# Kernel tuning notes

Measured on AMD Instinct MI355X. Metric: run time of the kernel, lower is better.

The kernel has to match this reference:

```python
import jax, jax.numpy as jnp
import numpy as np

B, S, D, A = 8, 4096, 128, 128


def _pos_encoding(seq_len, dim):
    # sin/cos positional encoding, same construction as the torch buffer
    pos = np.arange(seq_len, dtype=np.float32)[:, None]
    div = np.exp(np.arange(0, dim, 2, dtype=np.float32) * (-np.log(10000.0) / dim))
    pe = np.zeros((seq_len, dim), dtype=np.float32)
    pe[:, 0::2] = np.sin(pos * div)
    pe[:, 1::2] = np.cos(pos * div)
    return jnp.asarray(pe)


def setup_inputs() -> dict:
    key = jax.random.key(0)
    ks = jax.random.split(key, 7)
    sc = 1.0 / np.sqrt(D)
    return {
        "x": jax.random.normal(ks[0], (B, S, D), dtype=jnp.float32),
        "Wq": jax.random.normal(ks[1], (D, A), dtype=jnp.float32) * sc,
        "bq": jnp.zeros((A,), dtype=jnp.float32),
        "Wk": jax.random.normal(ks[2], (D, A), dtype=jnp.float32) * sc,
        "bk": jnp.zeros((A,), dtype=jnp.float32),
        "Wv": jax.random.normal(ks[3], (D, A), dtype=jnp.float32) * sc,
        "bv": jnp.zeros((A,), dtype=jnp.float32),
    }


def reference(x, Wq, bq, Wk, bk, Wv, bv):
    b, s, d = x.shape
    pe = _pos_encoding(s, d)  # [S, D]
    xp = x + pe[None]  # broadcast add of positional encoding
    q = xp @ Wq + bq  # [B, S, A]
    k = xp @ Wk + bk
    v = xp @ Wv + bv
    scale = 1.0 / jnp.sqrt(jnp.asarray(Wq.shape[1], dtype=jnp.float32))
    scores = jnp.einsum("bsa,bta->bst", q, k) * scale  # [B, S, S]
    weights = jax.nn.softmax(scores, axis=-1)
    out = jnp.einsum("bst,bta->bsa", weights, v)  # [B, S, A]
    return out
```

## Files before the change

### kernel.cpp

```cpp
#include <hip/hip_runtime.h>

#define BB 8
#define SS 4096
#define DD 128

typedef __attribute__((ext_vector_type(8))) short v8s;
typedef __attribute__((ext_vector_type(4))) float v4f;
typedef __attribute__((ext_vector_type(16))) float v16f;

__device__ __forceinline__ unsigned short f2bf(float f) {
    unsigned int u = __float_as_uint(f);
    u += 0x7fffu + ((u >> 16) & 1u);
    return (unsigned short)(u >> 16);
}
__device__ __forceinline__ unsigned int pk_bf16(float a, float b) {
    unsigned int ua = __float_as_uint(a) + 0x8000u;
    unsigned int ub = __float_as_uint(b) + 0x8000u;
    return __builtin_amdgcn_perm(ub, ua, 0x07060302u);
}

#if !defined(__HIP_DEVICE_COMPILE__)
#define MFMA16(a, b, c) (c)
#define MFMA32(a, b, c) (c)
#define GLDS16(g, l)
#define WAITVM(n)
#define WAITLGKM()
#define BAR()
#else
#define MFMA16(a, b, c) __builtin_amdgcn_mfma_f32_16x16x32_bf16((a), (b), (c), 0, 0, 0)
#define MFMA32(a, b, c) __builtin_amdgcn_mfma_f32_32x32x16_bf16((a), (b), (c), 0, 0, 0)
#define GLDS16(g, l)                                                         \
    __builtin_amdgcn_global_load_lds(                                        \
        (const __attribute__((address_space(1))) unsigned int*)(g),          \
        (__attribute__((address_space(3))) unsigned int*)(l), 16, 0, 0)
#define WAITVM(n) asm volatile("s_waitcnt vmcnt(" #n ")" ::: "memory")
#define WAITLGKM() asm volatile("s_waitcnt lgkmcnt(0)" ::: "memory")
#define BAR()                                                                \
    do {                                                                     \
        asm volatile("" ::: "memory");                                       \
        __builtin_amdgcn_s_barrier();                                        \
        __builtin_amdgcn_sched_barrier(0);                                   \
        asm volatile("" ::: "memory");                                       \
    } while (0)
#endif

#if !defined(__HIP_DEVICE_COMPILE__)
#define EXP2F(x) exp2f(x)
#elif __has_builtin(__builtin_amdgcn_exp2f)
#define EXP2F(x) __builtin_amdgcn_exp2f(x)
#else
#define EXP2F(x) exp2f(x)
#endif

#define QSCALE 0.12751743f

__global__ __launch_bounds__(256) void prep_kernel(
    const float* __restrict__ Wq, const float* __restrict__ Wk,
    const float* __restrict__ Wv, unsigned short* __restrict__ Wt)
{
    int id = blockIdx.x * 256 + threadIdx.x;
    int w = id >> 14;
    int n = (id >> 7) & 127;
    int k = id & 127;
    const float* W = (w == 0) ? Wq : (w == 1) ? Wk : Wv;
    Wt[id] = f2bf(W[k * 128 + n]);
}

__global__ __launch_bounds__(256, 3) void proj_kernel(
    const float* __restrict__ x, const unsigned short* __restrict__ Wt,
    const float* __restrict__ bq, const float* __restrict__ bk,
    const float* __restrict__ bv,
    unsigned short* __restrict__ qo, unsigned short* __restrict__ ko,
    unsigned short* __restrict__ vo)
{
    __shared__ __attribute__((aligned(16))) unsigned short w_lds[128 * 136];
    __shared__ __attribute__((aligned(16))) unsigned short o_lds[9216];

    const int tid = threadIdx.x;
    const int wave = tid >> 6;
    const int lane = tid & 63;
    const int quad = lane >> 4;
    const int l15 = lane & 15;
    const int bid = blockIdx.x;
    const int mat = bid % 3;
    const int rbase = (bid / 3) * 64;

    const unsigned short* Wp = Wt + (mat << 14);
#pragma unroll
    for (int it = 0; it < 8; ++it) {
        int id = it * 256 + tid;
        int n = id >> 4, c8 = id & 15;
        *(v8s*)(w_lds + n * 136 + c8 * 8) = *(const v8s*)(Wp + n * 128 + c8 * 8);
    }

    const int flatrow = rbase + wave * 16 + l15;
    const int srow = flatrow & 4095;
    v8s af[4];
#pragma unroll
    for (int kc = 0; kc < 4; ++kc) {
        const int kbase = kc * 32 + quad * 8;
        const v4f* xp = (const v4f*)(x + (size_t)flatrow * DD + kbase);
        v4f x0 = xp[0], x1 = xp[1];
        float p[8];
#pragma unroll
        for (int j = 0; j < 8; j += 2) {
            float freq = __expf((float)(kbase + j) * -0.07195578415606394f);
            float arg = (float)srow * freq;
            p[j] = __sinf(arg);
            p[j + 1] = __cosf(arg);
        }
        v8s a;
#pragma unroll
        for (int j = 0; j < 4; ++j) a[j] = (short)f2bf(x0[j] + p[j]);
#pragma unroll
        for (int j = 0; j < 4; ++j) a[4 + j] = (short)f2bf(x1[j] + p[4 + j]);
        af[kc] = a;
    }

    const float* bias = (mat == 0) ? bq : (mat == 1) ? bk : bv;
    const int quadp = ((quad & 1) << 1) | (quad >> 1);
    __syncthreads();

#pragma unroll
    for (int nb = 0; nb < 8; ++nb) {
        const int col = nb * 16 + l15;
        v4f acc = {0.f, 0.f, 0.f, 0.f};
#pragma unroll
        for (int kc = 0; kc < 4; ++kc) {
            v8s bf = *(const v8s*)(w_lds + col * 136 + kc * 32 + quad * 8);
            acc = MFMA16(af[kc], bf, acc);
        }
        float bval = bias[col];
#pragma unroll
        for (int reg = 0; reg < 4; ++reg) {
            float val = acc[reg] + bval;
            if (mat == 0) {
                int lr = wave * 16 + quad * 4 + reg;
                o_lds[lr * 136 + col] = f2bf(val * QSCALE);
            } else if (mat == 1) {
                int lr = wave * 16 + quad * 4 + reg;
                o_lds[lr * 136 + col] = f2bf(val);
            } else {
                int plr = wave * 16 + quadp * 4 + reg;
                o_lds[col * 72 + plr] = f2bf(val);
            }
        }
    }
    __syncthreads();

    if (mat <= 1) {
        unsigned short* outp = (mat == 0) ? qo : ko;
#pragma unroll
        for (int it = 0; it < 4; ++it) {
            int id = it * 256 + tid;
            int r = id >> 4, c8 = id & 15;
            *(v8s*)(outp + (size_t)(rbase + r) * DD + c8 * 8) =
                *(const v8s*)(o_lds + r * 136 + c8 * 8);
        }
    } else {
        const int b0 = rbase >> 12, s0 = rbase & 4095;
#pragma unroll
        for (int it = 0; it < 4; ++it) {
            int id = it * 256 + tid;
            int a = id >> 3, c = id & 7;
            *(v8s*)(vo + ((size_t)(b0 * 128 + a)) * SS + s0 + c * 8) =
                *(const v8s*)(o_lds + a * 72 + c * 8);
        }
    }
}

#define HKEYS 2048
#define NT 32
__global__ __launch_bounds__(512, 2) void flash_kernel(
    const unsigned short* __restrict__ qp,
    const unsigned short* __restrict__ kp,
    const unsigned short* __restrict__ vp,
    float* __restrict__ outp)
{
    __shared__ __attribute__((aligned(16))) unsigned short k_lds[2][2][8192];
    __shared__ __attribute__((aligned(16))) unsigned short v_lds[2][2][8192];
    __shared__ float xl[8][32];

    const int tid = threadIdx.x;
    const int wave = tid >> 6;
    const int lane = tid & 63;
    const int hi = lane >> 5;
    const int l31 = lane & 31;
    const int half = wave >> 2;
    const int qs = wave & 3;
    const int wv = wave & 3;
    const int bid = blockIdx.x;
    const int b = bid & 7;
    const int qt = bid >> 3;
    const int qbase = qt * 128;

    const size_t qrow = (size_t)(b * SS + qbase + qs * 32 + l31) * DD;
    v8s qf[8];
#pragma unroll
    for (int kc = 0; kc < 8; ++kc)
        qf[kc] = *(const v8s*)(qp + qrow + kc * 16 + hi * 8);

    v16f o[4];
#pragma unroll
    for (int fg = 0; fg < 4; ++fg)
#pragma unroll
        for (int r = 0; r < 16; ++r) o[fg][r] = 0.f;
    float lp = 0.f;

    const int kro = half * 32768 + l31 * 256 + ((hi ^ (l31 & 15)) << 4);
    const int vro = half * 32768 + l31 * 128 + (((l31 & 7) ^ hi) << 4);

    const int krow = wv * 4 + (lane >> 4);
    const unsigned short* ksrc =
        kp + ((size_t)(b * SS + half * HKEYS) + krow) * DD +
        (((lane & 15) ^ krow) << 3);
    const int vrow = lane >> 3;
    const unsigned short* vsrc =
        vp + (size_t)b * DD * SS + (size_t)(wv * 8 + vrow) * SS + half * HKEYS +
        (((lane & 7) ^ vrow) << 3);
    unsigned short* kd0 = &k_lds[half][0][wv * 512];
    unsigned short* vd0 = &v_lds[half][0][wv * 512];

    auto stage = [&](int p, int t) {
        unsigned short* kd = kd0 + p * 8192;
        unsigned short* vd = vd0 + p * 8192;
        const unsigned short* ks = ksrc + (size_t)t * 64 * DD;
        const unsigned short* vs = vsrc + t * 64;
#pragma unroll
        for (int it = 0; it < 4; ++it)
            GLDS16(ks + (size_t)it * 16 * DD, kd + it * 2048);
#pragma unroll
        for (int it = 0; it < 4; ++it)
            GLDS16(vs + (size_t)it * 32 * SS, vd + it * 2048);
    };

    auto compute = [&](int p, int sub) {
        const int ka = kro + p * 16384 + sub * 8192;
        v16f s;
#pragma unroll
        for (int r = 0; r < 16; ++r) s[r] = 0.f;
#pragma unroll
        for (int kc = 0; kc < 8; ++kc) {
            v8s af = *(const v8s*)((const char*)k_lds + (ka ^ (kc << 5)));
            s = MFMA32(af, qf[kc], s);
        }
        float e[16];
#pragma unroll
        for (int r = 0; r < 16; ++r) e[r] = EXP2F(s[r]);
        lp += (((e[0] + e[1]) + (e[2] + e[3])) + ((e[4] + e[5]) + (e[6] + e[7]))) +
              (((e[8] + e[9]) + (e[10] + e[11])) + ((e[12] + e[13]) + (e[14] + e[15])));
        union { v8s v[2]; unsigned int u[8]; } P;
#pragma unroll
        for (int g = 0; g < 2; ++g)
#pragma unroll
            for (int m = 0; m < 4; ++m)
                P.u[g * 4 + m] = pk_bf16(e[2 * m + 8 * g], e[2 * m + 8 * g + 1]);
        const int vb2 = (vro + p * 16384) ^ (sub << 6);
#pragma unroll
        for (int g = 0; g < 2; ++g) {
            const int vg = vb2 ^ (g << 5);
#pragma unroll
            for (int fg = 0; fg < 4; ++fg) {
                v8s bf = *(const v8s*)((const char*)v_lds + (vg + fg * 4096));
                o[fg] = MFMA32(P.v[g], bf, o[fg]);
            }
        }
    };

    stage(0, 0);
#pragma unroll 1
    for (int t = 0; t < NT; t += 2) {
        stage(1, t + 1);
        WAITVM(8);
        BAR();
        compute(0, 0);
        compute(0, 1);
        WAITLGKM();
        BAR();
        if (t + 2 < NT) {
            stage(0, t + 2);
            WAITVM(8);
        } else {
            WAITVM(0);
        }
        BAR();
        compute(1, 0);
        compute(1, 1);
        WAITLGKM();
        BAR();
    }

    lp += __shfl_xor(lp, 32);
    if (hi == 0) xl[wave][l31] = lp;

    float* kf = (float*)&k_lds[0][0][0];

    auto putO = [&](float* base) {
#pragma unroll
        for (int fg = 0; fg < 4; ++fg) {
            v4f* bp = (v4f*)(base + fg * 1024 + lane * 16);
#pragma unroll
            for (int c = 0; c < 4; ++c) {
                v4f tv = {o[fg][c * 4 + 0], o[fg][c * 4 + 1],
                          o[fg][c * 4 + 2], o[fg][c * 4 + 3]};
                bp[c ^ (lane & 3)] = tv;
            }
        }
    };
    auto addO = [&](const float* base) {
#pragma unroll
        for (int fg = 0; fg < 4; ++fg) {
            const v4f* bp = (const v4f*)(base + fg * 1024 + lane * 16);
#pragma unroll
            for (int c = 0; c < 4; ++c) {
                v4f tv = bp[c ^ (lane & 3)];
#pragma unroll
                for (int j = 0; j < 4; ++j) o[fg][c * 4 + j] += tv[j];
            }
        }
    };

    if (half == 1) putO(kf + qs * 4096);
    __syncthreads();
    if (half == 0) {
        addO(kf + qs * 4096);
        float ir[16];
#pragma unroll
        for (int r = 0; r < 16; ++r) {
            int qr = (r & 3) + 8 * (r >> 2) + 4 * hi;
            ir[r] = 1.0f / (xl[qs][qr] + xl[4 + qs][qr]);
        }
#pragma unroll
        for (int fg = 0; fg < 4; ++fg)
#pragma unroll
            for (int r = 0; r < 16; ++r) {
                int qr = (r & 3) + 8 * (r >> 2) + 4 * hi;
                outp[(size_t)(b * SS + qbase + qs * 32 + qr) * DD +
                     fg * 32 + l31] = o[fg][r] * ir[r];
            }
    }
}

extern "C" void kernel_launch(void* const* d_in, const int* in_sizes, int n_in,
                              void* d_out, int out_size, void* d_ws, size_t ws_size,
                              hipStream_t stream)
{
    const float* x  = (const float*)d_in[0];
    const float* Wq = (const float*)d_in[1];
    const float* bq = (const float*)d_in[2];
    const float* Wk = (const float*)d_in[3];
    const float* bk = (const float*)d_in[4];
    const float* Wv = (const float*)d_in[5];
    const float* bv = (const float*)d_in[6];
    float* out = (float*)d_out;

    unsigned short* Wt = (unsigned short*)d_ws;
    unsigned short* q  = Wt + 49152;
    unsigned short* k  = q + (size_t)BB * SS * DD;
    unsigned short* vT = k + (size_t)BB * SS * DD;

    hipLaunchKernelGGL(prep_kernel, dim3(192), dim3(256), 0, stream,
                       Wq, Wk, Wv, Wt);
    hipLaunchKernelGGL(proj_kernel, dim3(BB * SS / 64 * 3), dim3(256), 0, stream,
                       x, Wt, bq, bk, bv, q, k, vT);
    hipLaunchKernelGGL(flash_kernel, dim3(BB * SS / 128), dim3(512), 0, stream,
                       q, k, vT, out);
}
```

Measured before the change: 167.8 us.

## Fuse weight prep, QKV projection and flash attention into one kernel with grid barrier

Merges the three kernels into a single persistent launch. Each block projects its own 128 rows of Q, K and V, reading fp32 weights directly and transposing them into LDS. Q stays in swizzled LDS and is never written to global memory. K and V go to the workspace, and a software grid-wide atomic barrier makes them visible before attention starts. This removes launch gaps and the Q round-trip, but every block now repeats the weight conversion, and the barrier depends on all 256 blocks being co-resident.

```diff
diff --git a/kernel.cpp b/kernel.cpp
--- a/kernel.cpp
+++ b/kernel.cpp
@@ -54,151 +54,154 @@
 
 #define QSCALE 0.12751743f
 
-__global__ __launch_bounds__(256) void prep_kernel(
-    const float* __restrict__ Wq, const float* __restrict__ Wk,
-    const float* __restrict__ Wv, unsigned short* __restrict__ Wt)
-{
-    int id = blockIdx.x * 256 + threadIdx.x;
-    int w = id >> 14;
-    int n = (id >> 7) & 127;
-    int k = id & 127;
-    const float* W = (w == 0) ? Wq : (w == 1) ? Wk : Wv;
-    Wt[id] = f2bf(W[k * 128 + n]);
-}
-
-__global__ __launch_bounds__(256, 3) void proj_kernel(
-    const float* __restrict__ x, const unsigned short* __restrict__ Wt,
-    const float* __restrict__ bq, const float* __restrict__ bk,
-    const float* __restrict__ bv,
-    unsigned short* __restrict__ qo, unsigned short* __restrict__ ko,
-    unsigned short* __restrict__ vo)
-{
-    __shared__ __attribute__((aligned(16))) unsigned short w_lds[128 * 136];
-    __shared__ __attribute__((aligned(16))) unsigned short o_lds[9216];
-
-    const int tid = threadIdx.x;
-    const int wave = tid >> 6;
-    const int lane = tid & 63;
-    const int quad = lane >> 4;
-    const int l15 = lane & 15;
-    const int bid = blockIdx.x;
-    const int mat = bid % 3;
-    const int rbase = (bid / 3) * 64;
-
-    const unsigned short* Wp = Wt + (mat << 14);
-#pragma unroll
-    for (int it = 0; it < 8; ++it) {
-        int id = it * 256 + tid;
-        int n = id >> 4, c8 = id & 15;
-        *(v8s*)(w_lds + n * 136 + c8 * 8) = *(const v8s*)(Wp + n * 128 + c8 * 8);
-    }
-
-    const int flatrow = rbase + wave * 16 + l15;
-    const int srow = flatrow & 4095;
-    v8s af[4];
-#pragma unroll
-    for (int kc = 0; kc < 4; ++kc) {
-        const int kbase = kc * 32 + quad * 8;
-        const v4f* xp = (const v4f*)(x + (size_t)flatrow * DD + kbase);
-        v4f x0 = xp[0], x1 = xp[1];
-        float p[8];
-#pragma unroll
-        for (int j = 0; j < 8; j += 2) {
-            float freq = __expf((float)(kbase + j) * -0.07195578415606394f);
-            float arg = (float)srow * freq;
-            p[j] = __sinf(arg);
-            p[j + 1] = __cosf(arg);
-        }
-        v8s a;
-#pragma unroll
-        for (int j = 0; j < 4; ++j) a[j] = (short)f2bf(x0[j] + p[j]);
-#pragma unroll
-        for (int j = 0; j < 4; ++j) a[4 + j] = (short)f2bf(x1[j] + p[4 + j]);
-        af[kc] = a;
-    }
-
-    const float* bias = (mat == 0) ? bq : (mat == 1) ? bk : bv;
-    const int quadp = ((quad & 1) << 1) | (quad >> 1);
-    __syncthreads();
-
-#pragma unroll
-    for (int nb = 0; nb < 8; ++nb) {
-        const int col = nb * 16 + l15;
-        v4f acc = {0.f, 0.f, 0.f, 0.f};
-#pragma unroll
-        for (int kc = 0; kc < 4; ++kc) {
-            v8s bf = *(const v8s*)(w_lds + col * 136 + kc * 32 + quad * 8);
-            acc = MFMA16(af[kc], bf, acc);
-        }
-        float bval = bias[col];
-#pragma unroll
-        for (int reg = 0; reg < 4; ++reg) {
-            float val = acc[reg] + bval;
-            if (mat == 0) {
-                int lr = wave * 16 + quad * 4 + reg;
-                o_lds[lr * 136 + col] = f2bf(val * QSCALE);
-            } else if (mat == 1) {
-                int lr = wave * 16 + quad * 4 + reg;
-                o_lds[lr * 136 + col] = f2bf(val);
-            } else {
-                int plr = wave * 16 + quadp * 4 + reg;
-                o_lds[col * 72 + plr] = f2bf(val);
-            }
-        }
-    }
-    __syncthreads();
-
-    if (mat <= 1) {
-        unsigned short* outp = (mat == 0) ? qo : ko;
-#pragma unroll
-        for (int it = 0; it < 4; ++it) {
-            int id = it * 256 + tid;
-            int r = id >> 4, c8 = id & 15;
-            *(v8s*)(outp + (size_t)(rbase + r) * DD + c8 * 8) =
-                *(const v8s*)(o_lds + r * 136 + c8 * 8);
-        }
-    } else {
-        const int b0 = rbase >> 12, s0 = rbase & 4095;
-#pragma unroll
-        for (int it = 0; it < 4; ++it) {
-            int id = it * 256 + tid;
-            int a = id >> 3, c = id & 7;
-            *(v8s*)(vo + ((size_t)(b0 * 128 + a)) * SS + s0 + c * 8) =
-                *(const v8s*)(o_lds + a * 72 + c * 8);
-        }
-    }
-}
-
 #define HKEYS 2048
 #define NT 32
-__global__ __launch_bounds__(512, 2) void flash_kernel(
-    const unsigned short* __restrict__ qp,
-    const unsigned short* __restrict__ kp,
-    const unsigned short* __restrict__ vp,
-    float* __restrict__ outp)
+__global__ __launch_bounds__(512, 2) void fused_kernel(
+    const float* __restrict__ x,
+    const float* __restrict__ Wq, const float* __restrict__ bq,
+    const float* __restrict__ Wk, const float* __restrict__ bk,
+    const float* __restrict__ Wv, const float* __restrict__ bv,
+    unsigned short* __restrict__ ko, unsigned short* __restrict__ vo,
+    float* __restrict__ outp, unsigned int* bar)
 {
     __shared__ __attribute__((aligned(16))) unsigned short k_lds[2][2][8192];
     __shared__ __attribute__((aligned(16))) unsigned short v_lds[2][2][8192];
-    __shared__ float xl[8][32];
+    __shared__ __attribute__((aligned(16))) unsigned short q_lds[16384];
 
     const int tid = threadIdx.x;
     const int wave = tid >> 6;
     const int lane = tid & 63;
     const int hi = lane >> 5;
     const int l31 = lane & 31;
-    const int half = wave >> 2;
-    const int qs = wave & 3;
-    const int wv = wave & 3;
     const int bid = blockIdx.x;
     const int b = bid & 7;
     const int qt = bid >> 3;
     const int qbase = qt * 128;
 
-    const size_t qrow = (size_t)(b * SS + qbase + qs * 32 + l31) * DD;
+    {
+        const int quad = lane >> 4;
+        const int l15 = lane & 15;
+        const int xrow = qbase + wave * 16 + l15;
+
+        v8s af[4];
+#pragma unroll
+        for (int kc = 0; kc < 4; ++kc) {
+            const int kbase = kc * 32 + quad * 8;
+            const v4f* xp = (const v4f*)(x + (size_t)(b * SS + xrow) * DD + kbase);
+            v4f x0 = xp[0], x1 = xp[1];
+            float p[8];
+#pragma unroll
+            for (int j = 0; j < 8; j += 2) {
+                float freq = __expf((float)(kbase + j) * -0.07195578415606394f);
+                float arg = (float)xrow * freq;
+                p[j] = __sinf(arg);
+                p[j + 1] = __cosf(arg);
+            }
+            v8s a;
+#pragma unroll
+            for (int j = 0; j < 4; ++j) a[j] = (short)f2bf(x0[j] + p[j]);
+#pragma unroll
+            for (int j = 0; j < 4; ++j) a[4 + j] = (short)f2bf(x1[j] + p[4 + j]);
+            af[kc] = a;
+        }
+
+        unsigned short* w_lds = &k_lds[0][0][0];
+        unsigned short* o_lds = &v_lds[0][0][0];
+        const int quadp = ((quad & 1) << 1) | (quad >> 1);
+
+#pragma unroll 1
+        for (int m = 0; m < 3; ++m) {
+            const float* W = (m == 0) ? Wq : (m == 1) ? Wk : Wv;
+            const float* bias = (m == 0) ? bq : (m == 1) ? bk : bv;
+            __syncthreads();
+#pragma unroll
+            for (int j = 0; j < 32; ++j) {
+                int id = j * 512 + tid;
+                int n = id >> 7, k2 = id & 127;
+                w_lds[n * 136 + k2] = f2bf(W[k2 * 128 + n]);
+            }
+            __syncthreads();
+
+#pragma unroll
+            for (int nb = 0; nb < 8; ++nb) {
+                const int col = nb * 16 + l15;
+                v4f acc = {0.f, 0.f, 0.f, 0.f};
+#pragma unroll
+                for (int kc = 0; kc < 4; ++kc) {
+                    v8s bf = *(const v8s*)(w_lds + col * 136 + kc * 32 + quad * 8);
+                    acc = MFMA16(af[kc], bf, acc);
+                }
+                float bval = bias[col];
+#pragma unroll
+                for (int reg = 0; reg < 4; ++reg) {
+                    float val = acc[reg] + bval;
+                    if (m == 0) {
+                        int row = wave * 16 + quad * 4 + reg;
+                        int boff = row * 256 + ((col * 2) ^ ((row & 7) << 4));
+                        *(unsigned short*)((char*)q_lds + boff) =
+                            f2bf(val * QSCALE);
+                    } else if (m == 1) {
+                        int lr = wave * 16 + quad * 4 + reg;
+                        o_lds[lr * 136 + col] = f2bf(val);
+                    } else {
+                        int plr = wave * 16 + quadp * 4 + reg;
+                        o_lds[col * 136 + plr] = f2bf(val);
+                    }
+                }
+            }
+            if (m == 1) {
+                __syncthreads();
+#pragma unroll
+                for (int it = 0; it < 4; ++it) {
+                    int id = it * 512 + tid;
+                    int r = id >> 4, c8 = id & 15;
+                    *(v8s*)(ko + (size_t)(b * SS + qbase + r) * DD + c8 * 8) =
+                        *(const v8s*)(o_lds + r * 136 + c8 * 8);
+                }
+            } else if (m == 2) {
+                __syncthreads();
+#pragma unroll
+                for (int it = 0; it < 4; ++it) {
+                    int id = it * 512 + tid;
+                    int a = id >> 4, c = id & 15;
+                    *(v8s*)(vo + (size_t)(b * DD + a) * SS + qbase + c * 8) =
+                        *(const v8s*)(o_lds + a * 136 + c * 8);
+                }
+            }
+        }
+    }
+
+    WAITVM(0);
+    __syncthreads();
+    if (tid == 0) {
+        __threadfence();
+        unsigned int gen = __hip_atomic_load(&bar[1], __ATOMIC_RELAXED,
+                                             __HIP_MEMORY_SCOPE_AGENT);
+        unsigned int old = __hip_atomic_fetch_add(&bar[0], 1u, __ATOMIC_ACQ_REL,
+                                                  __HIP_MEMORY_SCOPE_AGENT);
+        if (old == 255u) {
+            __hip_atomic_store(&bar[0], 0u, __ATOMIC_RELAXED,
+                               __HIP_MEMORY_SCOPE_AGENT);
+            __hip_atomic_fetch_add(&bar[1], 1u, __ATOMIC_ACQ_REL,
+                                   __HIP_MEMORY_SCOPE_AGENT);
+        } else {
+            while (__hip_atomic_load(&bar[1], __ATOMIC_ACQUIRE,
+                                     __HIP_MEMORY_SCOPE_AGENT) == gen) {}
+        }
+        __threadfence();
+    }
+    __syncthreads();
+
+    const int half = wave >> 2;
+    const int qs = wave & 3;
+    const int wv = wave & 3;
+
+    const int qrow2 = qs * 32 + l31;
+    const char* qlp = (const char*)q_lds + qrow2 * 256;
     v8s qf[8];
 #pragma unroll
     for (int kc = 0; kc < 8; ++kc)
-        qf[kc] = *(const v8s*)(qp + qrow + kc * 16 + hi * 8);
+        qf[kc] = *(const v8s*)(qlp + (((2 * kc + hi) ^ (qrow2 & 7)) << 4));
 
     v16f o[4];
 #pragma unroll
@@ -212,11 +215,11 @@
 
     const int krow = wv * 4 + (lane >> 4);
     const unsigned short* ksrc =
-        kp + ((size_t)(b * SS + half * HKEYS) + krow) * DD +
+        ko + ((size_t)(b * SS + half * HKEYS) + krow) * DD +
         (((lane & 15) ^ krow) << 3);
     const int vrow = lane >> 3;
     const unsigned short* vsrc =
-        vp + (size_t)b * DD * SS + (size_t)(wv * 8 + vrow) * SS + half * HKEYS +
+        vo + (size_t)b * DD * SS + (size_t)(wv * 8 + vrow) * SS + half * HKEYS +
         (((lane & 7) ^ vrow) << 3);
     unsigned short* kd0 = &k_lds[half][0][wv * 512];
     unsigned short* vd0 = &v_lds[half][0][wv * 512];
@@ -291,7 +294,8 @@
     }
 
     lp += __shfl_xor(lp, 32);
-    if (hi == 0) xl[wave][l31] = lp;
+    float* xl = (float*)q_lds;
+    if (hi == 0) xl[wave * 32 + l31] = lp;
 
     float* kf = (float*)&k_lds[0][0][0];
 
@@ -328,7 +332,7 @@
 #pragma unroll
         for (int r = 0; r < 16; ++r) {
             int qr = (r & 3) + 8 * (r >> 2) + 4 * hi;
-            ir[r] = 1.0f / (xl[qs][qr] + xl[4 + qs][qr]);
+            ir[r] = 1.0f / (xl[qs * 32 + qr] + xl[(4 + qs) * 32 + qr]);
         }
 #pragma unroll
         for (int fg = 0; fg < 4; ++fg)
@@ -354,15 +358,11 @@
     const float* bv = (const float*)d_in[6];
     float* out = (float*)d_out;
 
-    unsigned short* Wt = (unsigned short*)d_ws;
-    unsigned short* q  = Wt + 49152;
-    unsigned short* k  = q + (size_t)BB * SS * DD;
-    unsigned short* vT = k + (size_t)BB * SS * DD;
-
-    hipLaunchKernelGGL(prep_kernel, dim3(192), dim3(256), 0, stream,
-                       Wq, Wk, Wv, Wt);
-    hipLaunchKernelGGL(proj_kernel, dim3(BB * SS / 64 * 3), dim3(256), 0, stream,
-                       x, Wt, bq, bk, bv, q, k, vT);
-    hipLaunchKernelGGL(flash_kernel, dim3(BB * SS / 128), dim3(512), 0, stream,
-                       q, k, vT, out);
+    unsigned short* ko = (unsigned short*)d_ws;
+    unsigned short* vo = ko + (size_t)BB * SS * DD;
+    unsigned int* bar = (unsigned int*)(vo + (size_t)BB * SS * DD);
+
+    hipMemsetAsync(bar, 0, 8, stream);
+    hipLaunchKernelGGL(fused_kernel, dim3(BB * SS / 128), dim3(512), 0, stream,
+                       x, Wq, bq, Wk, bk, Wv, bv, ko, vo, out, bar);
 }
```

Measured after the change: 205.5 us. 1.22x slower.

## Split flash key halves into separate blocks with global partial merge

Applied to the files above, without the earlier changes.

The flash kernel's two key-halves, which previously ran as 8 waves in one 512-thread block, now run as separate 256-thread blocks. The second-half block writes its partial O and row sums to global workspace and signals a flag, and the first-half block spin-waits on that flag before merging and normalizing. The projection kernel now computes Q, K and V in one block per row tile, which removes the recomputation of the positional encoding and x loads across three blocks. The inter-block spin wait risks deadlock or stalls if the paired block is not scheduled, and the partial results add global memory traffic.

```diff
diff --git a/kernel.cpp b/kernel.cpp
--- a/kernel.cpp
+++ b/kernel.cpp
@@ -66,7 +66,7 @@
     Wt[id] = f2bf(W[k * 128 + n]);
 }
 
-__global__ __launch_bounds__(256, 3) void proj_kernel(
+__global__ __launch_bounds__(256, 2) void proj_kernel(
     const float* __restrict__ x, const unsigned short* __restrict__ Wt,
     const float* __restrict__ bq, const float* __restrict__ bk,
     const float* __restrict__ bv,
@@ -81,17 +81,7 @@
     const int lane = tid & 63;
     const int quad = lane >> 4;
     const int l15 = lane & 15;
-    const int bid = blockIdx.x;
-    const int mat = bid % 3;
-    const int rbase = (bid / 3) * 64;
-
-    const unsigned short* Wp = Wt + (mat << 14);
-#pragma unroll
-    for (int it = 0; it < 8; ++it) {
-        int id = it * 256 + tid;
-        int n = id >> 4, c8 = id & 15;
-        *(v8s*)(w_lds + n * 136 + c8 * 8) = *(const v8s*)(Wp + n * 128 + c8 * 8);
-    }
+    const int rbase = blockIdx.x * 64;
 
     const int flatrow = rbase + wave * 16 + l15;
     const int srow = flatrow & 4095;
@@ -117,82 +107,96 @@
         af[kc] = a;
     }
 
-    const float* bias = (mat == 0) ? bq : (mat == 1) ? bk : bv;
     const int quadp = ((quad & 1) << 1) | (quad >> 1);
-    __syncthreads();
-
-#pragma unroll
-    for (int nb = 0; nb < 8; ++nb) {
-        const int col = nb * 16 + l15;
-        v4f acc = {0.f, 0.f, 0.f, 0.f};
-#pragma unroll
-        for (int kc = 0; kc < 4; ++kc) {
-            v8s bf = *(const v8s*)(w_lds + col * 136 + kc * 32 + quad * 8);
-            acc = MFMA16(af[kc], bf, acc);
-        }
-        float bval = bias[col];
-#pragma unroll
-        for (int reg = 0; reg < 4; ++reg) {
-            float val = acc[reg] + bval;
-            if (mat == 0) {
-                int lr = wave * 16 + quad * 4 + reg;
-                o_lds[lr * 136 + col] = f2bf(val * QSCALE);
-            } else if (mat == 1) {
-                int lr = wave * 16 + quad * 4 + reg;
-                o_lds[lr * 136 + col] = f2bf(val);
-            } else {
-                int plr = wave * 16 + quadp * 4 + reg;
-                o_lds[col * 72 + plr] = f2bf(val);
-            }
-        }
-    }
-    __syncthreads();
-
-    if (mat <= 1) {
-        unsigned short* outp = (mat == 0) ? qo : ko;
-#pragma unroll
-        for (int it = 0; it < 4; ++it) {
+
+#pragma unroll 1
+    for (int m = 0; m < 3; ++m) {
+        const float* bias = (m == 0) ? bq : (m == 1) ? bk : bv;
+        __syncthreads();
+        const unsigned short* Wp = Wt + (m << 14);
+#pragma unroll
+        for (int it = 0; it < 8; ++it) {
             int id = it * 256 + tid;
-            int r = id >> 4, c8 = id & 15;
-            *(v8s*)(outp + (size_t)(rbase + r) * DD + c8 * 8) =
-                *(const v8s*)(o_lds + r * 136 + c8 * 8);
-        }
-    } else {
-        const int b0 = rbase >> 12, s0 = rbase & 4095;
-#pragma unroll
-        for (int it = 0; it < 4; ++it) {
-            int id = it * 256 + tid;
-            int a = id >> 3, c = id & 7;
-            *(v8s*)(vo + ((size_t)(b0 * 128 + a)) * SS + s0 + c * 8) =
-                *(const v8s*)(o_lds + a * 72 + c * 8);
+            int n = id >> 4, c8 = id & 15;
+            *(v8s*)(w_lds + n * 136 + c8 * 8) = *(const v8s*)(Wp + n * 128 + c8 * 8);
+        }
+        __syncthreads();
+
+#pragma unroll
+        for (int nb = 0; nb < 8; ++nb) {
+            const int col = nb * 16 + l15;
+            v4f acc = {0.f, 0.f, 0.f, 0.f};
+#pragma unroll
+            for (int kc = 0; kc < 4; ++kc) {
+                v8s bf = *(const v8s*)(w_lds + col * 136 + kc * 32 + quad * 8);
+                acc = MFMA16(af[kc], bf, acc);
+            }
+            float bval = bias[col];
+#pragma unroll
+            for (int reg = 0; reg < 4; ++reg) {
+                float val = acc[reg] + bval;
+                if (m == 0) {
+                    int lr = wave * 16 + quad * 4 + reg;
+                    o_lds[lr * 136 + col] = f2bf(val * QSCALE);
+                } else if (m == 1) {
+                    int lr = wave * 16 + quad * 4 + reg;
+                    o_lds[lr * 136 + col] = f2bf(val);
+                } else {
+                    int plr = wave * 16 + quadp * 4 + reg;
+                    o_lds[col * 72 + plr] = f2bf(val);
+                }
+            }
+        }
+        __syncthreads();
+
+        if (m <= 1) {
+            unsigned short* outp = (m == 0) ? qo : ko;
+#pragma unroll
+            for (int it = 0; it < 4; ++it) {
+                int id = it * 256 + tid;
+                int r = id >> 4, c8 = id & 15;
+                *(v8s*)(outp + (size_t)(rbase + r) * DD + c8 * 8) =
+                    *(const v8s*)(o_lds + r * 136 + c8 * 8);
+            }
+        } else {
+            const int b0 = rbase >> 12, s0 = rbase & 4095;
+#pragma unroll
+            for (int it = 0; it < 4; ++it) {
+                int id = it * 256 + tid;
+                int a = id >> 3, c = id & 7;
+                *(v8s*)(vo + ((size_t)(b0 * 128 + a)) * SS + s0 + c * 8) =
+                    *(const v8s*)(o_lds + a * 72 + c * 8);
+            }
         }
     }
 }
 
 #define HKEYS 2048
 #define NT 32
-__global__ __launch_bounds__(512, 2) void flash_kernel(
+__global__ __launch_bounds__(256, 2) void flash_kernel(
     const unsigned short* __restrict__ qp,
     const unsigned short* __restrict__ kp,
     const unsigned short* __restrict__ vp,
+    float* __restrict__ op_part, float* __restrict__ lp_part,
+    unsigned int* __restrict__ flags,
     float* __restrict__ outp)
 {
-    __shared__ __attribute__((aligned(16))) unsigned short k_lds[2][2][8192];
-    __shared__ __attribute__((aligned(16))) unsigned short v_lds[2][2][8192];
-    __shared__ float xl[8][32];
+    __shared__ __attribute__((aligned(16))) unsigned short k_lds[2][8192];
+    __shared__ __attribute__((aligned(16))) unsigned short v_lds[2][8192];
+    __shared__ float xl[128];
 
     const int tid = threadIdx.x;
     const int wave = tid >> 6;
     const int lane = tid & 63;
     const int hi = lane >> 5;
     const int l31 = lane & 31;
-    const int half = wave >> 2;
-    const int qs = wave & 3;
-    const int wv = wave & 3;
     const int bid = blockIdx.x;
     const int b = bid & 7;
-    const int qt = bid >> 3;
+    const int half = (bid >> 3) & 1;
+    const int qt = bid >> 4;
     const int qbase = qt * 128;
+    const int qs = wave;
+    const int wv = wave;
 
     const size_t qrow = (size_t)(b * SS + qbase + qs * 32 + l31) * DD;
     v8s qf[8];
@@ -207,8 +211,8 @@
         for (int r = 0; r < 16; ++r) o[fg][r] = 0.f;
     float lp = 0.f;
 
-    const int kro = half * 32768 + l31 * 256 + ((hi ^ (l31 & 15)) << 4);
-    const int vro = half * 32768 + l31 * 128 + (((l31 & 7) ^ hi) << 4);
+    const int kro = l31 * 256 + ((hi ^ (l31 & 15)) << 4);
+    const int vro = l31 * 128 + (((l31 & 7) ^ hi) << 4);
 
     const int krow = wv * 4 + (lane >> 4);
     const unsigned short* ksrc =
@@ -218,8 +222,8 @@
     const unsigned short* vsrc =
         vp + (size_t)b * DD * SS + (size_t)(wv * 8 + vrow) * SS + half * HKEYS +
         (((lane & 7) ^ vrow) << 3);
-    unsigned short* kd0 = &k_lds[half][0][wv * 512];
-    unsigned short* vd0 = &v_lds[half][0][wv * 512];
+    unsigned short* kd0 = &k_lds[0][wv * 512];
+    unsigned short* vd0 = &v_lds[0][wv * 512];
 
     auto stage = [&](int p, int t) {
         unsigned short* kd = kd0 + p * 8192;
@@ -291,52 +295,48 @@
     }
 
     lp += __shfl_xor(lp, 32);
-    if (hi == 0) xl[wave][l31] = lp;
-
-    float* kf = (float*)&k_lds[0][0][0];
-
-    auto putO = [&](float* base) {
-#pragma unroll
-        for (int fg = 0; fg < 4; ++fg) {
-            v4f* bp = (v4f*)(base + fg * 1024 + lane * 16);
-#pragma unroll
-            for (int c = 0; c < 4; ++c) {
-                v4f tv = {o[fg][c * 4 + 0], o[fg][c * 4 + 1],
-                          o[fg][c * 4 + 2], o[fg][c * 4 + 3]};
-                bp[c ^ (lane & 3)] = tv;
-            }
-        }
-    };
-    auto addO = [&](const float* base) {
-#pragma unroll
-        for (int fg = 0; fg < 4; ++fg) {
-            const v4f* bp = (const v4f*)(base + fg * 1024 + lane * 16);
-#pragma unroll
-            for (int c = 0; c < 4; ++c) {
-                v4f tv = bp[c ^ (lane & 3)];
-#pragma unroll
-                for (int j = 0; j < 4; ++j) o[fg][c * 4 + j] += tv[j];
-            }
-        }
-    };
-
-    if (half == 1) putO(kf + qs * 4096);
-    __syncthreads();
-    if (half == 0) {
-        addO(kf + qs * 4096);
+    const int pairIdx = qt * 8 + b;
+    float* OP = op_part + (size_t)pairIdx * 16384;
+    float* LP = lp_part + pairIdx * 128;
+
+    if (half == 1) {
+#pragma unroll
+        for (int fg = 0; fg < 4; ++fg)
+#pragma unroll
+            for (int r = 0; r < 16; ++r) {
+                int qr = (r & 3) + 8 * (r >> 2) + 4 * hi;
+                OP[(qs * 32 + qr) * 128 + fg * 32 + l31] = o[fg][r];
+            }
+        if (hi == 0) LP[qs * 32 + l31] = lp;
+        WAITVM(0);
+        __syncthreads();
+        if (tid == 0) {
+            __threadfence();
+            __hip_atomic_store(&flags[pairIdx], 1u, __ATOMIC_RELEASE,
+                               __HIP_MEMORY_SCOPE_AGENT);
+        }
+    } else {
+        if (hi == 0) xl[qs * 32 + l31] = lp;
+        if (tid == 0) {
+            while (__hip_atomic_load(&flags[pairIdx], __ATOMIC_ACQUIRE,
+                                     __HIP_MEMORY_SCOPE_AGENT) == 0u)
+                __builtin_amdgcn_s_sleep(2);
+            __threadfence();
+        }
+        __syncthreads();
         float ir[16];
 #pragma unroll
         for (int r = 0; r < 16; ++r) {
             int qr = (r & 3) + 8 * (r >> 2) + 4 * hi;
-            ir[r] = 1.0f / (xl[qs][qr] + xl[4 + qs][qr]);
+            ir[r] = 1.0f / (xl[qs * 32 + qr] + LP[qs * 32 + qr]);
         }
 #pragma unroll
         for (int fg = 0; fg < 4; ++fg)
 #pragma unroll
             for (int r = 0; r < 16; ++r) {
                 int qr = (r & 3) + 8 * (r >> 2) + 4 * hi;
-                outp[(size_t)(b * SS + qbase + qs * 32 + qr) * DD +
-                     fg * 32 + l31] = o[fg][r] * ir[r];
+                outp[(size_t)(b * SS + qbase + qs * 32 + qr) * DD + fg * 32 + l31] =
+                    (o[fg][r] + OP[(qs * 32 + qr) * 128 + fg * 32 + l31]) * ir[r];
             }
     }
 }
@@ -358,11 +358,15 @@
     unsigned short* q  = Wt + 49152;
     unsigned short* k  = q + (size_t)BB * SS * DD;
     unsigned short* vT = k + (size_t)BB * SS * DD;
-
+    float* op_part = (float*)(vT + (size_t)BB * SS * DD);
+    float* lp_part = op_part + (size_t)256 * 16384;
+    unsigned int* flags = (unsigned int*)(lp_part + 32768);
+
+    hipMemsetAsync(flags, 0, 256 * sizeof(unsigned int), stream);
     hipLaunchKernelGGL(prep_kernel, dim3(192), dim3(256), 0, stream,
                        Wq, Wk, Wv, Wt);
-    hipLaunchKernelGGL(proj_kernel, dim3(BB * SS / 64 * 3), dim3(256), 0, stream,
+    hipLaunchKernelGGL(proj_kernel, dim3(BB * SS / 64), dim3(256), 0, stream,
                        x, Wt, bq, bk, bv, q, k, vT);
-    hipLaunchKernelGGL(flash_kernel, dim3(BB * SS / 128), dim3(512), 0, stream,
-                       q, k, vT, out);
-}
+    hipLaunchKernelGGL(flash_kernel, dim3(BB * SS / 64), dim3(256), 0, stream,
+                       q, k, vT, op_part, lp_part, flags, out);
+}
```

Result: slower. 201.3 us (+20.0%).

## Store K/V in MFMA fragment layout and load directly to registers in flash kernel

Applied to the files above, without the earlier changes.

The projection kernel now computes Q, K and V in one block per 64 rows, reusing the positional-encoded x fragments across all three weight matrices. It writes K and V in a pre-swizzled, fragment-ordered layout. The flash kernel drops the LDS staging, async global-to-LDS copies and barriers, and loads K/V fragments straight from global memory into registers with a two-stage register double buffer over 32-key tiles. This removes LDS traffic and synchronisation in the inner loop, at the cost of higher register pressure and reliance on L2/cache for K/V reuse across the waves that share the same keys.

```diff
diff --git a/kernel.cpp b/kernel.cpp
--- a/kernel.cpp
+++ b/kernel.cpp
@@ -22,26 +22,9 @@
 #if !defined(__HIP_DEVICE_COMPILE__)
 #define MFMA16(a, b, c) (c)
 #define MFMA32(a, b, c) (c)
-#define GLDS16(g, l)
-#define WAITVM(n)
-#define WAITLGKM()
-#define BAR()
 #else
 #define MFMA16(a, b, c) __builtin_amdgcn_mfma_f32_16x16x32_bf16((a), (b), (c), 0, 0, 0)
 #define MFMA32(a, b, c) __builtin_amdgcn_mfma_f32_32x32x16_bf16((a), (b), (c), 0, 0, 0)
-#define GLDS16(g, l)                                                         \
-    __builtin_amdgcn_global_load_lds(                                        \
-        (const __attribute__((address_space(1))) unsigned int*)(g),          \
-        (__attribute__((address_space(3))) unsigned int*)(l), 16, 0, 0)
-#define WAITVM(n) asm volatile("s_waitcnt vmcnt(" #n ")" ::: "memory")
-#define WAITLGKM() asm volatile("s_waitcnt lgkmcnt(0)" ::: "memory")
-#define BAR()                                                                \
-    do {                                                                     \
-        asm volatile("" ::: "memory");                                       \
-        __builtin_amdgcn_s_barrier();                                        \
-        __builtin_amdgcn_sched_barrier(0);                                   \
-        asm volatile("" ::: "memory");                                       \
-    } while (0)
 #endif
 
 #if !defined(__HIP_DEVICE_COMPILE__)
@@ -66,12 +49,12 @@
     Wt[id] = f2bf(W[k * 128 + n]);
 }
 
-__global__ __launch_bounds__(256, 3) void proj_kernel(
+__global__ __launch_bounds__(256, 2) void proj_kernel(
     const float* __restrict__ x, const unsigned short* __restrict__ Wt,
     const float* __restrict__ bq, const float* __restrict__ bk,
     const float* __restrict__ bv,
-    unsigned short* __restrict__ qo, unsigned short* __restrict__ ko,
-    unsigned short* __restrict__ vo)
+    unsigned short* __restrict__ qo, unsigned short* __restrict__ kF,
+    unsigned short* __restrict__ vF)
 {
     __shared__ __attribute__((aligned(16))) unsigned short w_lds[128 * 136];
     __shared__ __attribute__((aligned(16))) unsigned short o_lds[9216];
@@ -81,17 +64,7 @@
     const int lane = tid & 63;
     const int quad = lane >> 4;
     const int l15 = lane & 15;
-    const int bid = blockIdx.x;
-    const int mat = bid % 3;
-    const int rbase = (bid / 3) * 64;
-
-    const unsigned short* Wp = Wt + (mat << 14);
-#pragma unroll
-    for (int it = 0; it < 8; ++it) {
-        int id = it * 256 + tid;
-        int n = id >> 4, c8 = id & 15;
-        *(v8s*)(w_lds + n * 136 + c8 * 8) = *(const v8s*)(Wp + n * 128 + c8 * 8);
-    }
+    const int rbase = blockIdx.x * 64;
 
     const int flatrow = rbase + wave * 16 + l15;
     const int srow = flatrow & 4095;
@@ -117,69 +90,87 @@
         af[kc] = a;
     }
 
-    const float* bias = (mat == 0) ? bq : (mat == 1) ? bk : bv;
     const int quadp = ((quad & 1) << 1) | (quad >> 1);
-    __syncthreads();
-
-#pragma unroll
-    for (int nb = 0; nb < 8; ++nb) {
-        const int col = nb * 16 + l15;
-        v4f acc = {0.f, 0.f, 0.f, 0.f};
-#pragma unroll
-        for (int kc = 0; kc < 4; ++kc) {
-            v8s bf = *(const v8s*)(w_lds + col * 136 + kc * 32 + quad * 8);
-            acc = MFMA16(af[kc], bf, acc);
-        }
-        float bval = bias[col];
-#pragma unroll
-        for (int reg = 0; reg < 4; ++reg) {
-            float val = acc[reg] + bval;
-            if (mat == 0) {
-                int lr = wave * 16 + quad * 4 + reg;
-                o_lds[lr * 136 + col] = f2bf(val * QSCALE);
-            } else if (mat == 1) {
-                int lr = wave * 16 + quad * 4 + reg;
-                o_lds[lr * 136 + col] = f2bf(val);
-            } else {
-                int plr = wave * 16 + quadp * 4 + reg;
-                o_lds[col * 72 + plr] = f2bf(val);
+    const int b0 = rbase >> 12, s0 = rbase & 4095;
+    const size_t t0 = (size_t)b0 * 128 + (s0 >> 5);
+
+#pragma unroll 1
+    for (int m = 0; m < 3; ++m) {
+        const float* bias = (m == 0) ? bq : (m == 1) ? bk : bv;
+        __syncthreads();
+        const unsigned short* Wp = Wt + (m << 14);
+#pragma unroll
+        for (int it = 0; it < 8; ++it) {
+            int id = it * 256 + tid;
+            int n = id >> 4, c8 = id & 15;
+            *(v8s*)(w_lds + n * 136 + c8 * 8) = *(const v8s*)(Wp + n * 128 + c8 * 8);
+        }
+        __syncthreads();
+
+#pragma unroll
+        for (int nb = 0; nb < 8; ++nb) {
+            const int col = nb * 16 + l15;
+            v4f acc = {0.f, 0.f, 0.f, 0.f};
+#pragma unroll
+            for (int kc = 0; kc < 4; ++kc) {
+                v8s bf = *(const v8s*)(w_lds + col * 136 + kc * 32 + quad * 8);
+                acc = MFMA16(af[kc], bf, acc);
+            }
+            float bval = bias[col];
+#pragma unroll
+            for (int reg = 0; reg < 4; ++reg) {
+                float val = acc[reg] + bval;
+                if (m == 0) {
+                    int lr = wave * 16 + quad * 4 + reg;
+                    o_lds[lr * 136 + col] = f2bf(val * QSCALE);
+                } else if (m == 1) {
+                    int lr = wave * 16 + quad * 4 + reg;
+                    o_lds[lr * 136 + col] = f2bf(val);
+                } else {
+                    int plr = wave * 16 + quadp * 4 + reg;
+                    o_lds[col * 72 + plr] = f2bf(val);
+                }
+            }
+        }
+        __syncthreads();
+
+        if (m == 0) {
+#pragma unroll
+            for (int it = 0; it < 4; ++it) {
+                int id = it * 256 + tid;
+                int r = id >> 4, c8 = id & 15;
+                *(v8s*)(qo + (size_t)(rbase + r) * DD + c8 * 8) =
+                    *(const v8s*)(o_lds + r * 136 + c8 * 8);
+            }
+        } else if (m == 1) {
+#pragma unroll
+            for (int it = 0; it < 4; ++it) {
+                int id = it * 256 + tid;
+                int r = id & 63, c8 = id >> 6;
+                *(v8s*)(kF + (((t0 + (r >> 5)) * 16 + c8) * 32 + (r & 31)) * 8) =
+                    *(const v8s*)(o_lds + r * 136 + c8 * 8);
+            }
+        } else {
+#pragma unroll
+            for (int it = 0; it < 4; ++it) {
+                int id = it * 256 + tid;
+                int c = id >> 7, col = id & 127;
+                *(v8s*)(vF + (((t0 + (c >> 2)) * 4 + (c & 3)) * 128 + col) * 8) =
+                    *(const v8s*)(o_lds + col * 72 + c * 8);
             }
         }
     }
-    __syncthreads();
-
-    if (mat <= 1) {
-        unsigned short* outp = (mat == 0) ? qo : ko;
-#pragma unroll
-        for (int it = 0; it < 4; ++it) {
-            int id = it * 256 + tid;
-            int r = id >> 4, c8 = id & 15;
-            *(v8s*)(outp + (size_t)(rbase + r) * DD + c8 * 8) =
-                *(const v8s*)(o_lds + r * 136 + c8 * 8);
-        }
-    } else {
-        const int b0 = rbase >> 12, s0 = rbase & 4095;
-#pragma unroll
-        for (int it = 0; it < 4; ++it) {
-            int id = it * 256 + tid;
-            int a = id >> 3, c = id & 7;
-            *(v8s*)(vo + ((size_t)(b0 * 128 + a)) * SS + s0 + c * 8) =
-                *(const v8s*)(o_lds + a * 72 + c * 8);
-        }
-    }
-}
-
-#define HKEYS 2048
-#define NT 32
+}
+
+#define NT 64
 __global__ __launch_bounds__(512, 2) void flash_kernel(
     const unsigned short* __restrict__ qp,
-    const unsigned short* __restrict__ kp,
-    const unsigned short* __restrict__ vp,
+    const unsigned short* __restrict__ kF,
+    const unsigned short* __restrict__ vF,
     float* __restrict__ outp)
 {
-    __shared__ __attribute__((aligned(16))) unsigned short k_lds[2][2][8192];
-    __shared__ __attribute__((aligned(16))) unsigned short v_lds[2][2][8192];
-    __shared__ float xl[8][32];
+    __shared__ __attribute__((aligned(16))) float mrg[16384];
+    __shared__ float xl[8 * 32];
 
     const int tid = threadIdx.x;
     const int wave = tid >> 6;
@@ -188,7 +179,6 @@
     const int l31 = lane & 31;
     const int half = wave >> 2;
     const int qs = wave & 3;
-    const int wv = wave & 3;
     const int bid = blockIdx.x;
     const int b = bid & 7;
     const int qt = bid >> 3;
@@ -207,93 +197,66 @@
         for (int r = 0; r < 16; ++r) o[fg][r] = 0.f;
     float lp = 0.f;
 
-    const int kro = half * 32768 + l31 * 256 + ((hi ^ (l31 & 15)) << 4);
-    const int vro = half * 32768 + l31 * 128 + (((l31 & 7) ^ hi) << 4);
-
-    const int krow = wv * 4 + (lane >> 4);
-    const unsigned short* ksrc =
-        kp + ((size_t)(b * SS + half * HKEYS) + krow) * DD +
-        (((lane & 15) ^ krow) << 3);
-    const int vrow = lane >> 3;
-    const unsigned short* vsrc =
-        vp + (size_t)b * DD * SS + (size_t)(wv * 8 + vrow) * SS + half * HKEYS +
-        (((lane & 7) ^ vrow) << 3);
-    unsigned short* kd0 = &k_lds[half][0][wv * 512];
-    unsigned short* vd0 = &v_lds[half][0][wv * 512];
-
-    auto stage = [&](int p, int t) {
-        unsigned short* kd = kd0 + p * 8192;
-        unsigned short* vd = vd0 + p * 8192;
-        const unsigned short* ks = ksrc + (size_t)t * 64 * DD;
-        const unsigned short* vs = vsrc + t * 64;
-#pragma unroll
-        for (int it = 0; it < 4; ++it)
-            GLDS16(ks + (size_t)it * 16 * DD, kd + it * 2048);
-#pragma unroll
-        for (int it = 0; it < 4; ++it)
-            GLDS16(vs + (size_t)it * 32 * SS, vd + it * 2048);
-    };
-
-    auto compute = [&](int p, int sub) {
-        const int ka = kro + p * 16384 + sub * 8192;
+    const size_t tbase = ((size_t)(b * 128 + half * 64)) * 4096;
+    const unsigned short* kW = kF + tbase + hi * 256 + l31 * 8;
+    const unsigned short* vW = vF + tbase + hi * 1024 + l31 * 8;
+
+    v8s kfA[8], kfB[8], vf[8];
+    auto loadK = [&](v8s (&kf)[8], int t) {
+        const unsigned short* p = kW + (size_t)t * 4096;
+#pragma unroll
+        for (int kc = 0; kc < 8; ++kc)
+            kf[kc] = *(const v8s*)(p + kc * 512);
+    };
+    auto loadV = [&](int t) {
+        const unsigned short* p = vW + (size_t)t * 4096;
+#pragma unroll
+        for (int g = 0; g < 2; ++g)
+#pragma unroll
+            for (int fg = 0; fg < 4; ++fg)
+                vf[g * 4 + fg] = *(const v8s*)(p + g * 2048 + fg * 256);
+    };
+    auto qkpv = [&](const v8s (&kf)[8]) {
         v16f s;
 #pragma unroll
         for (int r = 0; r < 16; ++r) s[r] = 0.f;
 #pragma unroll
-        for (int kc = 0; kc < 8; ++kc) {
-            v8s af = *(const v8s*)((const char*)k_lds + (ka ^ (kc << 5)));
-            s = MFMA32(af, qf[kc], s);
-        }
-        float e[16];
-#pragma unroll
-        for (int r = 0; r < 16; ++r) e[r] = EXP2F(s[r]);
-        lp += (((e[0] + e[1]) + (e[2] + e[3])) + ((e[4] + e[5]) + (e[6] + e[7]))) +
-              (((e[8] + e[9]) + (e[10] + e[11])) + ((e[12] + e[13]) + (e[14] + e[15])));
+        for (int kc = 0; kc < 8; ++kc)
+            s = MFMA32(kf[kc], qf[kc], s);
         union { v8s v[2]; unsigned int u[8]; } P;
+        float sum = 0.f;
+#pragma unroll
+        for (int g2 = 0; g2 < 2; ++g2) {
+            float e[8];
+#pragma unroll
+            for (int r = 0; r < 8; ++r) e[r] = EXP2F(s[g2 * 8 + r]);
+            sum += ((e[0] + e[1]) + (e[2] + e[3])) +
+                   ((e[4] + e[5]) + (e[6] + e[7]));
+#pragma unroll
+            for (int m = 0; m < 4; ++m)
+                P.u[g2 * 4 + m] = pk_bf16(e[2 * m], e[2 * m + 1]);
+        }
+        lp += sum;
 #pragma unroll
         for (int g = 0; g < 2; ++g)
 #pragma unroll
-            for (int m = 0; m < 4; ++m)
-                P.u[g * 4 + m] = pk_bf16(e[2 * m + 8 * g], e[2 * m + 8 * g + 1]);
-        const int vb2 = (vro + p * 16384) ^ (sub << 6);
-#pragma unroll
-        for (int g = 0; g < 2; ++g) {
-            const int vg = vb2 ^ (g << 5);
-#pragma unroll
-            for (int fg = 0; fg < 4; ++fg) {
-                v8s bf = *(const v8s*)((const char*)v_lds + (vg + fg * 4096));
-                o[fg] = MFMA32(P.v[g], bf, o[fg]);
-            }
-        }
-    };
-
-    stage(0, 0);
+            for (int fg = 0; fg < 4; ++fg)
+                o[fg] = MFMA32(P.v[g], vf[g * 4 + fg], o[fg]);
+    };
+
+    loadK(kfA, 0);
 #pragma unroll 1
     for (int t = 0; t < NT; t += 2) {
-        stage(1, t + 1);
-        WAITVM(8);
-        BAR();
-        compute(0, 0);
-        compute(0, 1);
-        WAITLGKM();
-        BAR();
-        if (t + 2 < NT) {
-            stage(0, t + 2);
-            WAITVM(8);
-        } else {
-            WAITVM(0);
-        }
-        BAR();
-        compute(1, 0);
-        compute(1, 1);
-        WAITLGKM();
-        BAR();
+        loadV(t);
+        loadK(kfB, t + 1);
+        qkpv(kfA);
+        loadV(t + 1);
+        loadK(kfA, t + 2);
+        qkpv(kfB);
     }
 
     lp += __shfl_xor(lp, 32);
-    if (hi == 0) xl[wave][l31] = lp;
-
-    float* kf = (float*)&k_lds[0][0][0];
+    if (hi == 0) xl[wave * 32 + l31] = lp;
 
     auto putO = [&](float* base) {
 #pragma unroll
@@ -320,15 +283,15 @@
         }
     };
 
-    if (half == 1) putO(kf + qs * 4096);
+    if (half == 1) putO(mrg + qs * 4096);
     __syncthreads();
     if (half == 0) {
-        addO(kf + qs * 4096);
+        addO(mrg + qs * 4096);
         float ir[16];
 #pragma unroll
         for (int r = 0; r < 16; ++r) {
             int qr = (r & 3) + 8 * (r >> 2) + 4 * hi;
-            ir[r] = 1.0f / (xl[qs][qr] + xl[4 + qs][qr]);
+            ir[r] = 1.0f / (xl[qs * 32 + qr] + xl[(4 + qs) * 32 + qr]);
         }
 #pragma unroll
         for (int fg = 0; fg < 4; ++fg)
@@ -356,13 +319,13 @@
 
     unsigned short* Wt = (unsigned short*)d_ws;
     unsigned short* q  = Wt + 49152;
-    unsigned short* k  = q + (size_t)BB * SS * DD;
-    unsigned short* vT = k + (size_t)BB * SS * DD;
+    unsigned short* kF = q + (size_t)BB * SS * DD;
+    unsigned short* vF = kF + (size_t)BB * SS * DD;
 
     hipLaunchKernelGGL(prep_kernel, dim3(192), dim3(256), 0, stream,
                        Wq, Wk, Wv, Wt);
-    hipLaunchKernelGGL(proj_kernel, dim3(BB * SS / 64 * 3), dim3(256), 0, stream,
-                       x, Wt, bq, bk, bv, q, k, vT);
+    hipLaunchKernelGGL(proj_kernel, dim3(BB * SS / 64), dim3(256), 0, stream,
+                       x, Wt, bq, bk, bv, q, kF, vF);
     hipLaunchKernelGGL(flash_kernel, dim3(BB * SS / 128), dim3(512), 0, stream,
-                       q, k, vT, out);
-}
+                       q, kF, vF, out);
+}
```

Result: slower. 262.5 us (+56.5%).
